# Optimization experiments

Measured on AMD Instinct MI355X. Metric: run time of the kernel, lower is better.

The kernel has to match this reference:

```python
import jax, jax.numpy as jnp
import numpy as np

B, NB, S, D = 4096, 16, 256, 1024


def setup_inputs() -> dict:
    key = jax.random.key(0)
    k = jax.random.split(key, 6)
    sc_in = 1.0 / np.sqrt(D)
    sc_out = 1.0 / np.sqrt(S)
    return {
        "x": jax.random.normal(k[0], (B, D), dtype=jnp.float32),
        "y_index": jax.random.randint(k[1], (B, 1), 0, NB, dtype=jnp.int64),
        "W_in": jax.random.uniform(k[2], (NB, S, D), jnp.float32, -sc_in, sc_in),
        "b_in": jax.random.uniform(k[3], (NB, S), jnp.float32, -sc_in, sc_in),
        "W_out": jax.random.uniform(k[4], (NB, D, S), jnp.float32, -sc_out, sc_out),
        "b_out": jax.random.uniform(k[5], (NB, D), jnp.float32, -sc_out, sc_out),
    }


def reference(x, y_index, W_in, b_in, W_out, b_out):
    # h: [B, D] -> relu applied before every branch's fc_in (as in torch source)
    h = jax.nn.relu(x)
    # hiddens for all branches: [B, NB, S]
    hid = jnp.einsum("bd,nsd->bns", h, W_in) + b_in[None, :, :]
    # branch outputs stacked: [B, NB, D]
    outs = jnp.einsum("bns,nds->bnd", hid, W_out) + b_out[None, :, :]
    # gather selected branch per token: [B, D]
    sel = jnp.take_along_axis(outs, y_index[:, :, None], axis=1)[:, 0, :]
    return x + sel
```

## Files before the change

### kernel.cpp

```cpp
#include <hip/hip_runtime.h>


typedef unsigned short u16;
typedef short bf16x8 __attribute__((ext_vector_type(8)));
typedef float f32x4 __attribute__((ext_vector_type(4)));

#define MFMA16 __builtin_amdgcn_mfma_f32_16x16x32_bf16

constexpr int B_TOK = 4096;
constexpr int NB = 16;
constexpr int S_DIM = 256;
constexpr int D_DIM = 1024;
constexpr int BM = 64;
constexpr int PAD_ROWS = B_TOK + NB * BM;
constexpr int NTILES = PAD_ROWS / BM;

__device__ __forceinline__ unsigned short f2bf(float f) {
    unsigned u = __builtin_bit_cast(unsigned, f);
    u += 0x7fffu + ((u >> 16) & 1u);
    return (unsigned short)(u >> 16);
}
__device__ __forceinline__ unsigned pack2(float a, float b) {
    return (unsigned)f2bf(a) | ((unsigned)f2bf(b) << 16);
}
__device__ __forceinline__ void gload_lds16(const void* g, void* l) {
    __builtin_amdgcn_global_load_lds(
        (const __attribute__((address_space(1))) void*)g,
        (__attribute__((address_space(3))) void*)l, 16, 0, 0);
}

__global__ __launch_bounds__(256) void prep_kernel(
    const float* __restrict__ Wi_f, const float* __restrict__ Wo_f,
    u16* __restrict__ Wi, u16* __restrict__ Wo,
    const int* __restrict__ y, int* __restrict__ perm, int* __restrict__ tileBranch) {
    const int t = threadIdx.x;
    if (blockIdx.x == 0) {
        __shared__ int hist[NB];
        __shared__ int aoff[NB + 1];
        __shared__ int cursor[NB];
        if (t < NB) hist[t] = 0;
        __syncthreads();
        for (int i = t; i < B_TOK; i += 256) atomicAdd(&hist[y[i]], 1);
        __syncthreads();
        if (t == 0) {
            int off = 0;
            for (int n = 0; n < NB; ++n) {
                aoff[n] = off;
                cursor[n] = off;
                off += ((hist[n] + BM - 1) / BM) * BM;
            }
            aoff[NB] = off;
        }
        __syncthreads();
        for (int i = t; i < NTILES; i += 256) {
            int rb = i * BM, br = -1;
            for (int n = 0; n < NB; ++n)
                if (rb >= aoff[n] && rb < aoff[n + 1]) br = n;
            tileBranch[i] = br;
        }
        for (int i = t; i < PAD_ROWS; i += 256) perm[i] = -1;
        __syncthreads();
        for (int i = t; i < B_TOK; i += 256) {
            int pos = atomicAdd(&cursor[y[i]], 1);
            perm[pos] = i;
        }
        return;
    }
    int i = (blockIdx.x - 1) * 256 + t;
    const float* src;
    u16* dst;
    int j;
    if (i < 524288) { src = Wi_f; dst = Wi; j = i; }
    else            { src = Wo_f; dst = Wo; j = i - 524288; }
    const float4* p = (const float4*)src + (size_t)j * 2;
    float4 v0 = p[0], v1 = p[1];
    uint4 o;
    o.x = pack2(v0.x, v0.y);
    o.y = pack2(v0.z, v0.w);
    o.z = pack2(v1.x, v1.y);
    o.w = pack2(v1.z, v1.w);
    ((uint4*)dst)[j] = o;
}

__global__ __launch_bounds__(256) void gemm1_kernel(
    const float* __restrict__ x, const u16* __restrict__ Wi,
    const float* __restrict__ b_in, const int* __restrict__ tileBranch,
    const int* __restrict__ perm, u16* __restrict__ Hp) {
    const int branch = tileBranch[blockIdx.y];
    if (branch < 0) return;
    const int rowBase = blockIdx.y * BM;
    const int colBase = blockIdx.x * 128;

    __shared__ u16 sA[64 * 64];
    __shared__ u16 sB[128 * 64];

    const int t = threadIdx.x;
    const int ar = t >> 2;
    const int acg = t & 3;
    const int tok = perm[rowBase + ar];
    const float* aSrc = (tok >= 0) ? (x + (size_t)tok * D_DIM + acg * 16) : x;
    const int abyte0 = (ar * 128 + acg * 32) ^ ((ar & 7) << 4);
    const int abyte1 = (ar * 128 + acg * 32 + 16) ^ ((ar & 7) << 4);

    const u16* Bb = Wi + (size_t)branch * S_DIM * D_DIM + (size_t)colBase * D_DIM;

    const int lane = t & 63;
    const int wid = t >> 6;
    const int wm = (wid >> 1) * 32;
    const int wn = (wid & 1) * 64;
    const int fr = lane & 15;
    const int kc = (lane >> 4) << 3;

    f32x4 acc[2][4] = {};

    float4 v0, v1, v2, v3;
    {
        const float4* p = (const float4*)aSrc;
        v0 = p[0]; v1 = p[1]; v2 = p[2]; v3 = p[3];
    }

    for (int kt = 0; kt < 16; ++kt) {
        const int k0 = kt << 6;
#pragma unroll
        for (int i = 0; i < 4; ++i) {
            const int L = i * 4096 + t * 16;
            const int row = L >> 7;
            const int sunit = ((L >> 4) & 7) ^ (row & 7);
            const char* g = (const char*)Bb + (size_t)row * (D_DIM * 2) + k0 * 2 + sunit * 16;
            gload_lds16(g, (char*)sB + L);
        }
        uint4 w0, w1;
        if (tok >= 0) {
            w0.x = pack2(fmaxf(v0.x, 0.f), fmaxf(v0.y, 0.f));
            w0.y = pack2(fmaxf(v0.z, 0.f), fmaxf(v0.w, 0.f));
            w0.z = pack2(fmaxf(v1.x, 0.f), fmaxf(v1.y, 0.f));
            w0.w = pack2(fmaxf(v1.z, 0.f), fmaxf(v1.w, 0.f));
            w1.x = pack2(fmaxf(v2.x, 0.f), fmaxf(v2.y, 0.f));
            w1.y = pack2(fmaxf(v2.z, 0.f), fmaxf(v2.w, 0.f));
            w1.z = pack2(fmaxf(v3.x, 0.f), fmaxf(v3.y, 0.f));
            w1.w = pack2(fmaxf(v3.z, 0.f), fmaxf(v3.w, 0.f));
        } else {
            w0 = make_uint4(0, 0, 0, 0);
            w1 = make_uint4(0, 0, 0, 0);
        }
        *(uint4*)((char*)sA + abyte0) = w0;
        *(uint4*)((char*)sA + abyte1) = w1;
        if (kt < 15) {
            const float4* p = (const float4*)(aSrc + (k0 + 64));
            v0 = p[0]; v1 = p[1]; v2 = p[2]; v3 = p[3];
        }
        __syncthreads();
#pragma unroll
        for (int kk = 0; kk < 2; ++kk) {
            const int kcol = kc + kk * 32;
            const int ra0 = wm + fr, ra1 = wm + 16 + fr;
            bf16x8 a0 = *(const bf16x8*)&sA[(ra0 * 64 + kcol) ^ ((ra0 & 7) << 3)];
            bf16x8 a1 = *(const bf16x8*)&sA[(ra1 * 64 + kcol) ^ ((ra1 & 7) << 3)];
            bf16x8 b[4];
#pragma unroll
            for (int n = 0; n < 4; ++n) {
                const int rb = wn + n * 16 + fr;
                b[n] = *(const bf16x8*)&sB[(rb * 64 + kcol) ^ ((rb & 7) << 3)];
            }
#pragma unroll
            for (int n = 0; n < 4; ++n) {
                acc[0][n] = MFMA16(a0, b[n], acc[0][n], 0, 0, 0);
                acc[1][n] = MFMA16(a1, b[n], acc[1][n], 0, 0, 0);
            }
        }
        __syncthreads();
    }

    const int r0 = (lane >> 4) * 4;
#pragma unroll
    for (int m = 0; m < 2; ++m) {
        const int prow0 = rowBase + wm + m * 16 + r0;
#pragma unroll
        for (int n = 0; n < 4; ++n) {
            const int col = colBase + wn + n * 16 + fr;
            const float bv = b_in[branch * S_DIM + col];
#pragma unroll
            for (int r = 0; r < 4; ++r)
                Hp[(size_t)(prow0 + r) * S_DIM + col] = f2bf(acc[m][n][r] + bv);
        }
    }
}

__global__ __launch_bounds__(256) void gemm2_kernel(
    const u16* __restrict__ Hp, const u16* __restrict__ Wo,
    const float* __restrict__ b_out, const int* __restrict__ tileBranch,
    const int* __restrict__ perm, const float* __restrict__ x,
    float* __restrict__ out) {
    const int branch = tileBranch[blockIdx.y];
    if (branch < 0) return;
    const int rowBase = blockIdx.y * BM;
    const int colBase = blockIdx.x * 128;

    __shared__ u16 sA[64 * 64];
    __shared__ u16 sB[128 * 64];

    const int t = threadIdx.x;
    const u16* Ab = Hp + (size_t)rowBase * S_DIM;
    const u16* Bb = Wo + (size_t)branch * D_DIM * S_DIM + (size_t)colBase * S_DIM;

    const int lane = t & 63;
    const int wid = t >> 6;
    const int wm = (wid >> 1) * 32;
    const int wn = (wid & 1) * 64;
    const int fr = lane & 15;
    const int kc = (lane >> 4) << 3;

    f32x4 acc[2][4] = {};

    for (int kt = 0; kt < 4; ++kt) {
        const int k0 = kt << 6;
#pragma unroll
        for (int i = 0; i < 2; ++i) {
            const int L = i * 4096 + t * 16;
            const int row = L >> 7;
            const int sunit = ((L >> 4) & 7) ^ (row & 7);
            const char* g = (const char*)Ab + (size_t)row * (S_DIM * 2) + k0 * 2 + sunit * 16;
            gload_lds16(g, (char*)sA + L);
        }
#pragma unroll
        for (int i = 0; i < 4; ++i) {
            const int L = i * 4096 + t * 16;
            const int row = L >> 7;
            const int sunit = ((L >> 4) & 7) ^ (row & 7);
            const char* g = (const char*)Bb + (size_t)row * (S_DIM * 2) + k0 * 2 + sunit * 16;
            gload_lds16(g, (char*)sB + L);
        }
        __syncthreads();
#pragma unroll
        for (int kk = 0; kk < 2; ++kk) {
            const int kcol = kc + kk * 32;
            const int ra0 = wm + fr, ra1 = wm + 16 + fr;
            bf16x8 a0 = *(const bf16x8*)&sA[(ra0 * 64 + kcol) ^ ((ra0 & 7) << 3)];
            bf16x8 a1 = *(const bf16x8*)&sA[(ra1 * 64 + kcol) ^ ((ra1 & 7) << 3)];
            bf16x8 b[4];
#pragma unroll
            for (int n = 0; n < 4; ++n) {
                const int rb = wn + n * 16 + fr;
                b[n] = *(const bf16x8*)&sB[(rb * 64 + kcol) ^ ((rb & 7) << 3)];
            }
#pragma unroll
            for (int n = 0; n < 4; ++n) {
                acc[0][n] = MFMA16(a0, b[n], acc[0][n], 0, 0, 0);
                acc[1][n] = MFMA16(a1, b[n], acc[1][n], 0, 0, 0);
            }
        }
        __syncthreads();
    }

    const int r0 = (lane >> 4) * 4;
#pragma unroll
    for (int m = 0; m < 2; ++m) {
        const int prow0 = rowBase + wm + m * 16 + r0;
#pragma unroll
        for (int r = 0; r < 4; ++r) {
            const int tok = perm[prow0 + r];
            if (tok < 0) continue;
#pragma unroll
            for (int n = 0; n < 4; ++n) {
                const int col = colBase + wn + n * 16 + fr;
                const size_t o = (size_t)tok * D_DIM + col;
                out[o] = x[o] + acc[m][n][r] + b_out[branch * D_DIM + col];
            }
        }
    }
}

extern "C" void kernel_launch(void* const* d_in, const int* in_sizes, int n_in,
                              void* d_out, int out_size, void* d_ws, size_t ws_size,
                              hipStream_t stream) {
    const float* x     = (const float*)d_in[0];
    const int*   y     = (const int*)d_in[1];
    const float* W_in  = (const float*)d_in[2];
    const float* b_in  = (const float*)d_in[3];
    const float* W_out = (const float*)d_in[4];
    const float* b_out = (const float*)d_in[5];
    float* out = (float*)d_out;

    char* ws = (char*)d_ws;
    u16* Wi = (u16*)(ws);
    u16* Wo = (u16*)(ws + 8388608);
    u16* Hp = (u16*)(ws + 16777216);
    int* perm = (int*)(ws + 19398656);
    int* tileBranch = (int*)(ws + 19419136);

    prep_kernel<<<4097, 256, 0, stream>>>(W_in, W_out, Wi, Wo, y, perm, tileBranch);

    gemm1_kernel<<<dim3(S_DIM / 128, NTILES), 256, 0, stream>>>(
        x, Wi, b_in, tileBranch, perm, Hp);

    gemm2_kernel<<<dim3(D_DIM / 128, NTILES), 256, 0, stream>>>(
        Hp, Wo, b_out, tileBranch, perm, x, out);
}
```

Measured before the change: 57.32 us.

## Double-buffer LDS in both GEMMs, shrink gemm1 N tile, stage gemm2 epilogue

```diff
diff --git a/kernel.cpp b/kernel.cpp
--- a/kernel.cpp
+++ b/kernel.cpp
@@ -27,6 +27,10 @@
     __builtin_amdgcn_global_load_lds(
         (const __attribute__((address_space(1))) void*)g,
         (__attribute__((address_space(3))) void*)l, 16, 0, 0);
+}
+__device__ __forceinline__ void publish() {
+    asm volatile("s_waitcnt vmcnt(0)" ::: "memory");
+    __syncthreads();
 }
 
 __global__ __launch_bounds__(256) void prep_kernel(
@@ -89,10 +93,10 @@
     const int branch = tileBranch[blockIdx.y];
     if (branch < 0) return;
     const int rowBase = blockIdx.y * BM;
-    const int colBase = blockIdx.x * 128;
-
-    __shared__ u16 sA[64 * 64];
-    __shared__ u16 sB[128 * 64];
+    const int colBase = blockIdx.x * 64;
+
+    __shared__ u16 sA[2][64 * 64];
+    __shared__ u16 sB[2][64 * 64];
 
     const int t = threadIdx.x;
     const int ar = t >> 2;
@@ -100,35 +104,30 @@
     const int tok = perm[rowBase + ar];
     const float* aSrc = (tok >= 0) ? (x + (size_t)tok * D_DIM + acg * 16) : x;
     const int abyte0 = (ar * 128 + acg * 32) ^ ((ar & 7) << 4);
-    const int abyte1 = (ar * 128 + acg * 32 + 16) ^ ((ar & 7) << 4);
+    const int abyte1 = abyte0 ^ 16;
 
     const u16* Bb = Wi + (size_t)branch * S_DIM * D_DIM + (size_t)colBase * D_DIM;
 
     const int lane = t & 63;
     const int wid = t >> 6;
     const int wm = (wid >> 1) * 32;
-    const int wn = (wid & 1) * 64;
+    const int wn = (wid & 1) * 32;
     const int fr = lane & 15;
     const int kc = (lane >> 4) << 3;
 
-    f32x4 acc[2][4] = {};
-
-    float4 v0, v1, v2, v3;
-    {
-        const float4* p = (const float4*)aSrc;
-        v0 = p[0]; v1 = p[1]; v2 = p[2]; v3 = p[3];
-    }
-
-    for (int kt = 0; kt < 16; ++kt) {
-        const int k0 = kt << 6;
-#pragma unroll
-        for (int i = 0; i < 4; ++i) {
+    f32x4 acc[2][2] = {};
+
+    auto stageB = [&](int buf, int k0) {
+#pragma unroll
+        for (int i = 0; i < 2; ++i) {
             const int L = i * 4096 + t * 16;
             const int row = L >> 7;
             const int sunit = ((L >> 4) & 7) ^ (row & 7);
-            const char* g = (const char*)Bb + (size_t)row * (D_DIM * 2) + k0 * 2 + sunit * 16;
-            gload_lds16(g, (char*)sB + L);
-        }
+            gload_lds16((const char*)Bb + (size_t)row * (D_DIM * 2) + k0 * 2 + sunit * 16,
+                        (char*)sB[buf] + L);
+        }
+    };
+    auto packWriteA = [&](int buf, float4 v0, float4 v1, float4 v2, float4 v3) {
         uint4 w0, w1;
         if (tok >= 0) {
             w0.x = pack2(fmaxf(v0.x, 0.f), fmaxf(v0.y, 0.f));
@@ -143,32 +142,43 @@
             w0 = make_uint4(0, 0, 0, 0);
             w1 = make_uint4(0, 0, 0, 0);
         }
-        *(uint4*)((char*)sA + abyte0) = w0;
-        *(uint4*)((char*)sA + abyte1) = w1;
+        *(uint4*)((char*)sA[buf] + abyte0) = w0;
+        *(uint4*)((char*)sA[buf] + abyte1) = w1;
+    };
+
+    float4 v0, v1, v2, v3;
+    {
+        const float4* p = (const float4*)aSrc;
+        v0 = p[0]; v1 = p[1]; v2 = p[2]; v3 = p[3];
+    }
+    stageB(0, 0);
+    packWriteA(0, v0, v1, v2, v3);
+    publish();
+
+    for (int kt = 0; kt < 16; ++kt) {
+        const int cur = kt & 1;
         if (kt < 15) {
-            const float4* p = (const float4*)(aSrc + (k0 + 64));
+            const int k0n = (kt + 1) << 6;
+            stageB(cur ^ 1, k0n);
+            const float4* p = (const float4*)(aSrc + k0n);
             v0 = p[0]; v1 = p[1]; v2 = p[2]; v3 = p[3];
         }
-        __syncthreads();
 #pragma unroll
         for (int kk = 0; kk < 2; ++kk) {
             const int kcol = kc + kk * 32;
             const int ra0 = wm + fr, ra1 = wm + 16 + fr;
-            bf16x8 a0 = *(const bf16x8*)&sA[(ra0 * 64 + kcol) ^ ((ra0 & 7) << 3)];
-            bf16x8 a1 = *(const bf16x8*)&sA[(ra1 * 64 + kcol) ^ ((ra1 & 7) << 3)];
-            bf16x8 b[4];
-#pragma unroll
-            for (int n = 0; n < 4; ++n) {
-                const int rb = wn + n * 16 + fr;
-                b[n] = *(const bf16x8*)&sB[(rb * 64 + kcol) ^ ((rb & 7) << 3)];
-            }
-#pragma unroll
-            for (int n = 0; n < 4; ++n) {
-                acc[0][n] = MFMA16(a0, b[n], acc[0][n], 0, 0, 0);
-                acc[1][n] = MFMA16(a1, b[n], acc[1][n], 0, 0, 0);
-            }
-        }
-        __syncthreads();
+            const int rb0 = wn + fr, rb1 = wn + 16 + fr;
+            bf16x8 a0 = *(const bf16x8*)&sA[cur][(ra0 * 64 + kcol) ^ ((ra0 & 7) << 3)];
+            bf16x8 a1 = *(const bf16x8*)&sA[cur][(ra1 * 64 + kcol) ^ ((ra1 & 7) << 3)];
+            bf16x8 b0 = *(const bf16x8*)&sB[cur][(rb0 * 64 + kcol) ^ ((rb0 & 7) << 3)];
+            bf16x8 b1 = *(const bf16x8*)&sB[cur][(rb1 * 64 + kcol) ^ ((rb1 & 7) << 3)];
+            acc[0][0] = MFMA16(a0, b0, acc[0][0], 0, 0, 0);
+            acc[0][1] = MFMA16(a0, b1, acc[0][1], 0, 0, 0);
+            acc[1][0] = MFMA16(a1, b0, acc[1][0], 0, 0, 0);
+            acc[1][1] = MFMA16(a1, b1, acc[1][1], 0, 0, 0);
+        }
+        if (kt < 15) packWriteA(cur ^ 1, v0, v1, v2, v3);
+        publish();
     }
 
     const int r0 = (lane >> 4) * 4;
@@ -176,7 +186,7 @@
     for (int m = 0; m < 2; ++m) {
         const int prow0 = rowBase + wm + m * 16 + r0;
 #pragma unroll
-        for (int n = 0; n < 4; ++n) {
+        for (int n = 0; n < 2; ++n) {
             const int col = colBase + wn + n * 16 + fr;
             const float bv = b_in[branch * S_DIM + col];
 #pragma unroll
@@ -196,8 +206,11 @@
     const int rowBase = blockIdx.y * BM;
     const int colBase = blockIdx.x * 128;
 
-    __shared__ u16 sA[64 * 64];
-    __shared__ u16 sB[128 * 64];
+    __shared__ __align__(16) char smem[49152];
+    u16* sA0 = (u16*)smem;
+    u16* sA1 = (u16*)(smem + 8192);
+    u16* sB0 = (u16*)(smem + 16384);
+    u16* sB1 = (u16*)(smem + 32768);
 
     const int t = threadIdx.x;
     const u16* Ab = Hp + (size_t)rowBase * S_DIM;
@@ -212,36 +225,36 @@
 
     f32x4 acc[2][4] = {};
 
-    for (int kt = 0; kt < 4; ++kt) {
-        const int k0 = kt << 6;
+    auto stage = [&](u16* dA, u16* dB, int k0) {
 #pragma unroll
         for (int i = 0; i < 2; ++i) {
             const int L = i * 4096 + t * 16;
             const int row = L >> 7;
             const int sunit = ((L >> 4) & 7) ^ (row & 7);
-            const char* g = (const char*)Ab + (size_t)row * (S_DIM * 2) + k0 * 2 + sunit * 16;
-            gload_lds16(g, (char*)sA + L);
+            gload_lds16((const char*)Ab + (size_t)row * (S_DIM * 2) + k0 * 2 + sunit * 16,
+                        (char*)dA + L);
         }
 #pragma unroll
         for (int i = 0; i < 4; ++i) {
             const int L = i * 4096 + t * 16;
             const int row = L >> 7;
             const int sunit = ((L >> 4) & 7) ^ (row & 7);
-            const char* g = (const char*)Bb + (size_t)row * (S_DIM * 2) + k0 * 2 + sunit * 16;
-            gload_lds16(g, (char*)sB + L);
-        }
-        __syncthreads();
+            gload_lds16((const char*)Bb + (size_t)row * (S_DIM * 2) + k0 * 2 + sunit * 16,
+                        (char*)dB + L);
+        }
+    };
+    auto compute = [&](const u16* cA, const u16* cB) {
 #pragma unroll
         for (int kk = 0; kk < 2; ++kk) {
             const int kcol = kc + kk * 32;
             const int ra0 = wm + fr, ra1 = wm + 16 + fr;
-            bf16x8 a0 = *(const bf16x8*)&sA[(ra0 * 64 + kcol) ^ ((ra0 & 7) << 3)];
-            bf16x8 a1 = *(const bf16x8*)&sA[(ra1 * 64 + kcol) ^ ((ra1 & 7) << 3)];
+            bf16x8 a0 = *(const bf16x8*)&cA[(ra0 * 64 + kcol) ^ ((ra0 & 7) << 3)];
+            bf16x8 a1 = *(const bf16x8*)&cA[(ra1 * 64 + kcol) ^ ((ra1 & 7) << 3)];
             bf16x8 b[4];
 #pragma unroll
             for (int n = 0; n < 4; ++n) {
                 const int rb = wn + n * 16 + fr;
-                b[n] = *(const bf16x8*)&sB[(rb * 64 + kcol) ^ ((rb & 7) << 3)];
+                b[n] = *(const bf16x8*)&cB[(rb * 64 + kcol) ^ ((rb & 7) << 3)];
             }
 #pragma unroll
             for (int n = 0; n < 4; ++n) {
@@ -249,23 +262,49 @@
                 acc[1][n] = MFMA16(a1, b[n], acc[1][n], 0, 0, 0);
             }
         }
-        __syncthreads();
-    }
-
+    };
+
+    stage(sA0, sB0, 0);
+    publish();
+#pragma unroll
+    for (int kt = 0; kt < 4; ++kt) {
+        const bool even = (kt & 1) == 0;
+        if (kt < 3) stage(even ? sA1 : sA0, even ? sB1 : sB0, (kt + 1) << 6);
+        compute(even ? sA0 : sA1, even ? sB0 : sB1);
+        publish();
+    }
+
+    float* bo = (float*)smem;
     const int r0 = (lane >> 4) * 4;
 #pragma unroll
-    for (int m = 0; m < 2; ++m) {
-        const int prow0 = rowBase + wm + m * 16 + r0;
-#pragma unroll
-        for (int r = 0; r < 4; ++r) {
-            const int tok = perm[prow0 + r];
-            if (tok < 0) continue;
-#pragma unroll
-            for (int n = 0; n < 4; ++n) {
-                const int col = colBase + wn + n * 16 + fr;
-                const size_t o = (size_t)tok * D_DIM + col;
-                out[o] = x[o] + acc[m][n][r] + b_out[branch * D_DIM + col];
-            }
+    for (int m = 0; m < 2; ++m)
+#pragma unroll
+        for (int n = 0; n < 4; ++n)
+#pragma unroll
+            for (int r = 0; r < 4; ++r)
+                bo[(wm + m * 16 + r0 + r) * 132 + wn + n * 16 + fr] = acc[m][n][r];
+    __syncthreads();
+
+    const int brow = t >> 2;
+    const int q4 = (t & 3) * 4;
+    const int tok2 = perm[rowBase + brow];
+    if (tok2 >= 0) {
+        const size_t gbase = (size_t)tok2 * D_DIM + colBase;
+        const float* xr = x + gbase;
+        float* orow = out + gbase;
+        const float* br = b_out + (size_t)branch * D_DIM + colBase;
+#pragma unroll
+        for (int j = 0; j < 8; ++j) {
+            const int c = q4 + j * 16;
+            float4 xv = *(const float4*)&xr[c];
+            float4 bv = *(const float4*)&br[c];
+            float4 hv = *(const float4*)&bo[brow * 132 + c];
+            float4 s;
+            s.x = xv.x + bv.x + hv.x;
+            s.y = xv.y + bv.y + hv.y;
+            s.z = xv.z + bv.z + hv.z;
+            s.w = xv.w + bv.w + hv.w;
+            *(float4*)&orow[c] = s;
         }
     }
 }
@@ -290,7 +329,7 @@
 
     prep_kernel<<<4097, 256, 0, stream>>>(W_in, W_out, Wi, Wo, y, perm, tileBranch);
 
-    gemm1_kernel<<<dim3(S_DIM / 128, NTILES), 256, 0, stream>>>(
+    gemm1_kernel<<<dim3(S_DIM / 64, NTILES), 256, 0, stream>>>(
         x, Wi, b_in, tileBranch, perm, Hp);
 
     gemm2_kernel<<<dim3(D_DIM / 128, NTILES), 256, 0, stream>>>(
```

After: 55.24 us. 1.04x faster.
